# Performance work log

Hardware: AMD Instinct MI355X
Metric: run time of the kernel (lower is better)

The kernel has to match this reference:

```python
import jax, jax.numpy as jnp
import numpy as np

M = 4096   # out_features
N = 4096   # in_features
K_NNZ = 204  # nnz per row -> keep_ratio ~ 0.05
T = 8192   # tokens (batch*seq)


def setup_inputs() -> dict:
    key = jax.random.key(0)
    k1, k2, k3, k4 = jax.random.split(key, 4)
    # CSR structure: K_NNZ unique sorted columns per row (constant index buffers)
    rng = np.random.default_rng(0)
    cols = np.argsort(rng.random((M, N)), axis=1)[:, :K_NNZ]
    cols = np.sort(cols, axis=1).astype(np.int32)
    col_idx = jnp.asarray(cols.reshape(-1))                      # [nnz]
    row_ids = jnp.asarray(np.repeat(np.arange(M, dtype=np.int32), K_NNZ))  # [nnz]
    x = jax.random.normal(k1, (T, N), dtype=jnp.float32)
    dense_weight = jax.random.normal(k2, (M, N), dtype=jnp.float32) * 0.02
    bias = jax.random.normal(k3, (M,), dtype=jnp.float32) * 0.02
    sparse_values = jax.random.normal(k4, (M * K_NNZ,), dtype=jnp.float32) * 0.02
    return {"x": x, "dense_weight": dense_weight, "bias": bias,
            "sparse_values": sparse_values, "row_ids": row_ids, "col_idx": col_idx}


def reference(x, dense_weight, bias, sparse_values, row_ids, col_idx):
    # sp_add: scatter CSR values into the frozen dense weight (W = W_dense + W_sparse)
    W = dense_weight.at[row_ids, col_idx].add(sparse_values)     # [M, N]
    # sp_mm hot path: y = x @ W^T + b
    return jnp.dot(x, W.T) + bias                                # [T, M]
```

## Files before the change

kernel.cpp:

```cpp
#include <hip/hip_runtime.h>


typedef __attribute__((ext_vector_type(8))) __bf16 bf16x8;
typedef __attribute__((ext_vector_type(4))) float f32x4;
typedef __attribute__((ext_vector_type(8))) unsigned short u16x8;

#define BARRIER()   asm volatile("s_barrier" ::: "memory")
#define WAITLGKM0() asm volatile("s_waitcnt lgkmcnt(0)" ::: "memory")
#define WAITVM0()   asm volatile("s_waitcnt vmcnt(0)" ::: "memory")
#define SCHED0()    __builtin_amdgcn_sched_barrier(0)

__device__ __forceinline__ unsigned short f2bf(float f) {
  unsigned int u = __builtin_bit_cast(unsigned int, f);
  u += 0x7FFFu + ((u >> 16) & 1u);
  return (unsigned short)(u >> 16);
}

__global__ __launch_bounds__(256) void cvt_f32_bf16(
    const float* __restrict__ s, unsigned short* __restrict__ d, long n8) {
  long i = (long)blockIdx.x * blockDim.x + threadIdx.x;
  const long stride = (long)gridDim.x * blockDim.x;
  for (; i < n8; i += stride) {
    const float4* sp = (const float4*)(s + i * 8);
    float4 a = sp[0];
    float4 b = sp[1];
    u16x8 o;
    o[0] = f2bf(a.x); o[1] = f2bf(a.y); o[2] = f2bf(a.z); o[3] = f2bf(a.w);
    o[4] = f2bf(b.x); o[5] = f2bf(b.y); o[6] = f2bf(b.z); o[7] = f2bf(b.w);
    *(u16x8*)(d + i * 8) = o;
  }
}

__global__ __launch_bounds__(256) void sparse_scatter(
    const float* __restrict__ dense, const float* __restrict__ vals,
    const int* __restrict__ rows, const int* __restrict__ cols,
    unsigned short* __restrict__ Wb, int nnz, int K) {
  int i = blockIdx.x * blockDim.x + threadIdx.x;
  if (i < nnz) {
    size_t off = (size_t)rows[i] * (size_t)K + (size_t)cols[i];
    Wb[off] = f2bf(dense[off] + vals[i]);
  }
}

__global__ __launch_bounds__(512, 2) void gemm256f(
    const unsigned short* __restrict__ A,
    const unsigned short* __restrict__ B,
    const float* __restrict__ bias,
    float* __restrict__ C,
    int Tm, int Mn, int K) {
  extern __shared__ __align__(16) char smem[];

  const int tid  = threadIdx.x;
  const int lane = tid & 63;
  const int wid  = tid >> 6;
  const int wm = (wid >> 2) * 128;
  const int wn = (wid & 3) * 64;

  const int nwg = gridDim.x;
  int bid = blockIdx.x;
  if ((nwg & 7) == 0) bid = (bid & 7) * (nwg >> 3) + (bid >> 3);
  const int ntn = Mn >> 8;
  const int bm0 = (bid / ntn) << 8;
  const int bn0 = (bid % ntn) << 8;

  const int NT = K >> 6;

  const int sr  = tid >> 3;
  const int gq8 = ((tid & 7) ^ (sr & 7)) * 8;
  const unsigned short* Asrc = A + (size_t)(bm0 + sr) * K + gq8;
  const unsigned short* Bsrc = B + (size_t)(bn0 + sr) * K + gq8;
  const size_t r64 = (size_t)64 * K;
  const int ldst = tid * 16;

#define STAGEH(SRC, H, LDSB, KOFF) do {                                          \
    __builtin_amdgcn_global_load_lds(                                            \
      (const __attribute__((address_space(1))) void*)((SRC) + (size_t)(H)*2*r64 + (KOFF)), \
      (__attribute__((address_space(3))) void*)(smem + (LDSB) + ldst), 16, 0, 0);\
    __builtin_amdgcn_global_load_lds(                                            \
      (const __attribute__((address_space(1))) void*)((SRC) + (size_t)(H)*2*r64 + r64 + (KOFF)), \
      (__attribute__((address_space(3))) void*)(smem + (LDSB) + 8192 + ldst), 16, 0, 0); \
  } while (0)

  const int fr = lane & 15, cq = lane >> 4;
  const int f7 = fr & 7;
  const int q0 = ((cq ^ f7) << 4);
  const int q1 = (((4 + cq) ^ f7) << 4);
  const int arow = (wm + fr) * 128;
  const int brow = (wn + fr) * 128;

  f32x4 acc[8][4] = {};
  bf16x8 aq0[4], aq1[4], bA0[2], bA1[2], bB0[2], bB1[2];

  STAGEH(Asrc, 0, 0, 0);
  STAGEH(Asrc, 1, 16384, 0);
  STAGEH(Bsrc, 0, 32768, 0);
  STAGEH(Bsrc, 1, 49152, 0);
  WAITVM0();
  BARRIER();

#pragma unroll 2
  for (int t = 0; t < NT; ++t) {
    const char* Ab = smem + (t & 1) * 65536;
    const char* Bb = Ab + 32768;
    const int nbase = ((t & 1) ^ 1) * 65536;
    const int kn = (t + 1) * 64;

    if (t + 1 < NT) {
      STAGEH(Asrc, 0, nbase, kn);
      STAGEH(Asrc, 1, nbase + 16384, kn);
      STAGEH(Bsrc, 0, nbase + 32768, kn);
      STAGEH(Bsrc, 1, nbase + 49152, kn);
    }

#pragma unroll
    for (int m = 0; m < 4; ++m) {
      aq0[m] = *(const bf16x8*)(Ab + arow + m * 2048 + q0);
      aq1[m] = *(const bf16x8*)(Ab + arow + m * 2048 + q1);
    }
#pragma unroll
    for (int n = 0; n < 2; ++n) {
      bA0[n] = *(const bf16x8*)(Bb + brow + n * 2048 + q0);
      bA1[n] = *(const bf16x8*)(Bb + brow + n * 2048 + q1);
    }
    WAITLGKM0();
    SCHED0();
    __builtin_amdgcn_s_setprio(1);
#pragma unroll
    for (int m = 0; m < 4; ++m)
#pragma unroll
      for (int n = 0; n < 2; ++n) {
        acc[m][n] = __builtin_amdgcn_mfma_f32_16x16x32_bf16(aq0[m], bA0[n], acc[m][n], 0, 0, 0);
        acc[m][n] = __builtin_amdgcn_mfma_f32_16x16x32_bf16(aq1[m], bA1[n], acc[m][n], 0, 0, 0);
      }
    __builtin_amdgcn_s_setprio(0);
    SCHED0();

#pragma unroll
    for (int n = 0; n < 2; ++n) {
      bB0[n] = *(const bf16x8*)(Bb + brow + (n + 2) * 2048 + q0);
      bB1[n] = *(const bf16x8*)(Bb + brow + (n + 2) * 2048 + q1);
    }
    WAITLGKM0();
    SCHED0();
    __builtin_amdgcn_s_setprio(1);
#pragma unroll
    for (int m = 0; m < 4; ++m)
#pragma unroll
      for (int n = 0; n < 2; ++n) {
        acc[m][n + 2] = __builtin_amdgcn_mfma_f32_16x16x32_bf16(aq0[m], bB0[n], acc[m][n + 2], 0, 0, 0);
        acc[m][n + 2] = __builtin_amdgcn_mfma_f32_16x16x32_bf16(aq1[m], bB1[n], acc[m][n + 2], 0, 0, 0);
      }
    __builtin_amdgcn_s_setprio(0);
    SCHED0();

#pragma unroll
    for (int m = 0; m < 4; ++m) {
      aq0[m] = *(const bf16x8*)(Ab + arow + (m + 4) * 2048 + q0);
      aq1[m] = *(const bf16x8*)(Ab + arow + (m + 4) * 2048 + q1);
    }
    WAITLGKM0();
    SCHED0();
    __builtin_amdgcn_s_setprio(1);
#pragma unroll
    for (int m = 0; m < 4; ++m)
#pragma unroll
      for (int n = 0; n < 2; ++n) {
        acc[m + 4][n] = __builtin_amdgcn_mfma_f32_16x16x32_bf16(aq0[m], bA0[n], acc[m + 4][n], 0, 0, 0);
        acc[m + 4][n] = __builtin_amdgcn_mfma_f32_16x16x32_bf16(aq1[m], bA1[n], acc[m + 4][n], 0, 0, 0);
      }
    __builtin_amdgcn_s_setprio(0);
    SCHED0();

    __builtin_amdgcn_s_setprio(1);
#pragma unroll
    for (int m = 0; m < 4; ++m)
#pragma unroll
      for (int n = 0; n < 2; ++n) {
        acc[m + 4][n + 2] = __builtin_amdgcn_mfma_f32_16x16x32_bf16(aq0[m], bB0[n], acc[m + 4][n + 2], 0, 0, 0);
        acc[m + 4][n + 2] = __builtin_amdgcn_mfma_f32_16x16x32_bf16(aq1[m], bB1[n], acc[m + 4][n + 2], 0, 0, 0);
      }
    __builtin_amdgcn_s_setprio(0);
    WAITVM0();
    BARRIER();
  }
#undef STAGEH

  const int c4 = cq * 4;
#pragma unroll
  for (int n = 0; n < 4; ++n) {
    const int col = bn0 + wn + n * 16 + fr;
    const float bv = bias[col];
#pragma unroll
    for (int m = 0; m < 8; ++m) {
      const size_t rowb = (size_t)(bm0 + wm + m * 16 + c4);
#pragma unroll
      for (int q = 0; q < 4; ++q)
        C[(rowb + q) * (size_t)Mn + col] = acc[m][n][q] + bv;
    }
  }
}

extern "C" void kernel_launch(void* const* d_in, const int* in_sizes, int n_in,
                              void* d_out, int out_size, void* d_ws, size_t ws_size,
                              hipStream_t stream) {
  const float* x     = (const float*)d_in[0];
  const float* dw    = (const float*)d_in[1];
  const float* bias  = (const float*)d_in[2];
  const float* sv    = (const float*)d_in[3];
  const int*   rows  = (const int*)d_in[4];
  const int*   cols  = (const int*)d_in[5];
  float* out = (float*)d_out;

  const int  Mn = in_sizes[2];
  const long wElems = (long)in_sizes[1];
  const int  K  = (int)(wElems / Mn);
  const long xElems = (long)in_sizes[0];
  const int  Tm = (int)(xElems / K);
  const int  nnz = in_sizes[3];

  unsigned short* Wb = (unsigned short*)d_ws;
  unsigned short* Xb = Wb + wElems;

  cvt_f32_bf16<<<2048, 256, 0, stream>>>(dw, Wb, wElems / 8);
  sparse_scatter<<<(nnz + 255) / 256, 256, 0, stream>>>(dw, sv, rows, cols, Wb, nnz, K);
  cvt_f32_bf16<<<2048, 256, 0, stream>>>(x, Xb, xElems / 8);

  dim3 grid((Tm >> 8) * (Mn >> 8));
  gemm256f<<<grid, 512, 131072, stream>>>(Xb, Wb, bias, out, Tm, Mn, K);
}
```

Measured before the change: 302.5 us.

## Use four waves with 128x128 warp tiles and interleave staging with LDS reads

The GEMM workgroup drops from 8 waves to 4. Each wave now computes a 128x128 output tile with an 8x8 accumulator array, which raises register reuse per LDS fragment read. Global-to-LDS staging for the next K tile is split into A and B halves, issued between fragment reads, and the explicit lgkmcnt waits and priority hints are removed. This relies on compiler-inserted waits, and the 256 accumulator VGPRs plus fragments may push register pressure high or cause spills while halving the waves available per CU.

```diff
diff --git a/kernel.cpp b/kernel.cpp
--- a/kernel.cpp
+++ b/kernel.cpp
@@ -6,7 +6,6 @@
 typedef __attribute__((ext_vector_type(8))) unsigned short u16x8;
 
 #define BARRIER()   asm volatile("s_barrier" ::: "memory")
-#define WAITLGKM0() asm volatile("s_waitcnt lgkmcnt(0)" ::: "memory")
 #define WAITVM0()   asm volatile("s_waitcnt vmcnt(0)" ::: "memory")
 #define SCHED0()    __builtin_amdgcn_sched_barrier(0)
 
@@ -42,7 +41,7 @@
   }
 }
 
-__global__ __launch_bounds__(512, 2) void gemm256f(
+__global__ __launch_bounds__(256, 1) void gemm4w(
     const unsigned short* __restrict__ A,
     const unsigned short* __restrict__ B,
     const float* __restrict__ bias,
@@ -53,8 +52,8 @@
   const int tid  = threadIdx.x;
   const int lane = tid & 63;
   const int wid  = tid >> 6;
-  const int wm = (wid >> 2) * 128;
-  const int wn = (wid & 3) * 64;
+  const int wm = (wid >> 1) * 128;
+  const int wn = (wid & 1) * 128;
 
   const int nwg = gridDim.x;
   int bid = blockIdx.x;
@@ -69,16 +68,16 @@
   const int gq8 = ((tid & 7) ^ (sr & 7)) * 8;
   const unsigned short* Asrc = A + (size_t)(bm0 + sr) * K + gq8;
   const unsigned short* Bsrc = B + (size_t)(bn0 + sr) * K + gq8;
-  const size_t r64 = (size_t)64 * K;
+  const size_t r32 = (size_t)32 * K;
   const int ldst = tid * 16;
 
-#define STAGEH(SRC, H, LDSB, KOFF) do {                                          \
-    __builtin_amdgcn_global_load_lds(                                            \
-      (const __attribute__((address_space(1))) void*)((SRC) + (size_t)(H)*2*r64 + (KOFF)), \
-      (__attribute__((address_space(3))) void*)(smem + (LDSB) + ldst), 16, 0, 0);\
-    __builtin_amdgcn_global_load_lds(                                            \
-      (const __attribute__((address_space(1))) void*)((SRC) + (size_t)(H)*2*r64 + r64 + (KOFF)), \
-      (__attribute__((address_space(3))) void*)(smem + (LDSB) + 8192 + ldst), 16, 0, 0); \
+#define STAGE8(SRC, LDSB, KOFF) do {                                             \
+    _Pragma("unroll")                                                            \
+    for (int c = 0; c < 8; ++c)                                                  \
+      __builtin_amdgcn_global_load_lds(                                          \
+        (const __attribute__((address_space(1))) void*)((SRC) + (size_t)c * r32 + (KOFF)), \
+        (__attribute__((address_space(3))) void*)(smem + (LDSB) + c * 4096 + ldst), \
+        16, 0, 0);                                                               \
   } while (0)
 
   const int fr = lane & 15, cq = lane >> 4;
@@ -88,13 +87,11 @@
   const int arow = (wm + fr) * 128;
   const int brow = (wn + fr) * 128;
 
-  f32x4 acc[8][4] = {};
-  bf16x8 aq0[4], aq1[4], bA0[2], bA1[2], bB0[2], bB1[2];
+  f32x4 acc[8][8] = {};
+  bf16x8 a0[8], a1[8], b0[8], b1[8];
 
-  STAGEH(Asrc, 0, 0, 0);
-  STAGEH(Asrc, 1, 16384, 0);
-  STAGEH(Bsrc, 0, 32768, 0);
-  STAGEH(Bsrc, 1, 49152, 0);
+  STAGE8(Asrc, 0, 0);
+  STAGE8(Bsrc, 32768, 0);
   WAITVM0();
   BARRIER();
 
@@ -104,90 +101,51 @@
     const char* Bb = Ab + 32768;
     const int nbase = ((t & 1) ^ 1) * 65536;
     const int kn = (t + 1) * 64;
-
-    if (t + 1 < NT) {
-      STAGEH(Asrc, 0, nbase, kn);
-      STAGEH(Asrc, 1, nbase + 16384, kn);
-      STAGEH(Bsrc, 0, nbase + 32768, kn);
-      STAGEH(Bsrc, 1, nbase + 49152, kn);
-    }
+    const bool st = (t + 1 < NT);
 
 #pragma unroll
-    for (int m = 0; m < 4; ++m) {
-      aq0[m] = *(const bf16x8*)(Ab + arow + m * 2048 + q0);
-      aq1[m] = *(const bf16x8*)(Ab + arow + m * 2048 + q1);
-    }
+    for (int m = 0; m < 8; ++m)
+      a0[m] = *(const bf16x8*)(Ab + arow + m * 2048 + q0);
 #pragma unroll
-    for (int n = 0; n < 2; ++n) {
-      bA0[n] = *(const bf16x8*)(Bb + brow + n * 2048 + q0);
-      bA1[n] = *(const bf16x8*)(Bb + brow + n * 2048 + q1);
-    }
-    WAITLGKM0();
+    for (int n = 0; n < 8; ++n)
+      b0[n] = *(const bf16x8*)(Bb + brow + n * 2048 + q0);
     SCHED0();
-    __builtin_amdgcn_s_setprio(1);
-#pragma unroll
-    for (int m = 0; m < 4; ++m)
-#pragma unroll
-      for (int n = 0; n < 2; ++n) {
-        acc[m][n] = __builtin_amdgcn_mfma_f32_16x16x32_bf16(aq0[m], bA0[n], acc[m][n], 0, 0, 0);
-        acc[m][n] = __builtin_amdgcn_mfma_f32_16x16x32_bf16(aq1[m], bA1[n], acc[m][n], 0, 0, 0);
-      }
-    __builtin_amdgcn_s_setprio(0);
+
+    if (st) STAGE8(Asrc, nbase, kn);
     SCHED0();
 
 #pragma unroll
-    for (int n = 0; n < 2; ++n) {
-      bB0[n] = *(const bf16x8*)(Bb + brow + (n + 2) * 2048 + q0);
-      bB1[n] = *(const bf16x8*)(Bb + brow + (n + 2) * 2048 + q1);
-    }
-    WAITLGKM0();
+    for (int m = 0; m < 8; ++m)
+      a1[m] = *(const bf16x8*)(Ab + arow + m * 2048 + q1);
+#pragma unroll
+    for (int n = 0; n < 8; ++n)
+      b1[n] = *(const bf16x8*)(Bb + brow + n * 2048 + q1);
     SCHED0();
-    __builtin_amdgcn_s_setprio(1);
-#pragma unroll
-    for (int m = 0; m < 4; ++m)
-#pragma unroll
-      for (int n = 0; n < 2; ++n) {
-        acc[m][n + 2] = __builtin_amdgcn_mfma_f32_16x16x32_bf16(aq0[m], bB0[n], acc[m][n + 2], 0, 0, 0);
-        acc[m][n + 2] = __builtin_amdgcn_mfma_f32_16x16x32_bf16(aq1[m], bB1[n], acc[m][n + 2], 0, 0, 0);
-      }
-    __builtin_amdgcn_s_setprio(0);
+
+    if (st) STAGE8(Bsrc, nbase + 32768, kn);
     SCHED0();
 
 #pragma unroll
-    for (int m = 0; m < 4; ++m) {
-      aq0[m] = *(const bf16x8*)(Ab + arow + (m + 4) * 2048 + q0);
-      aq1[m] = *(const bf16x8*)(Ab + arow + (m + 4) * 2048 + q1);
-    }
-    WAITLGKM0();
-    SCHED0();
-    __builtin_amdgcn_s_setprio(1);
+    for (int m = 0; m < 8; ++m)
 #pragma unroll
-    for (int m = 0; m < 4; ++m)
-#pragma unroll
-      for (int n = 0; n < 2; ++n) {
-        acc[m + 4][n] = __builtin_amdgcn_mfma_f32_16x16x32_bf16(aq0[m], bA0[n], acc[m + 4][n], 0, 0, 0);
-        acc[m + 4][n] = __builtin_amdgcn_mfma_f32_16x16x32_bf16(aq1[m], bA1[n], acc[m + 4][n], 0, 0, 0);
-      }
-    __builtin_amdgcn_s_setprio(0);
+      for (int n = 0; n < 8; ++n)
+        acc[m][n] = __builtin_amdgcn_mfma_f32_16x16x32_bf16(a0[m], b0[n], acc[m][n], 0, 0, 0);
     SCHED0();
 
-    __builtin_amdgcn_s_setprio(1);
 #pragma unroll
-    for (int m = 0; m < 4; ++m)
+    for (int m = 0; m < 8; ++m)
 #pragma unroll
-      for (int n = 0; n < 2; ++n) {
-        acc[m + 4][n + 2] = __builtin_amdgcn_mfma_f32_16x16x32_bf16(aq0[m], bB0[n], acc[m + 4][n + 2], 0, 0, 0);
-        acc[m + 4][n + 2] = __builtin_amdgcn_mfma_f32_16x16x32_bf16(aq1[m], bB1[n], acc[m + 4][n + 2], 0, 0, 0);
-      }
-    __builtin_amdgcn_s_setprio(0);
+      for (int n = 0; n < 8; ++n)
+        acc[m][n] = __builtin_amdgcn_mfma_f32_16x16x32_bf16(a1[m], b1[n], acc[m][n], 0, 0, 0);
+
     WAITVM0();
     BARRIER();
   }
-#undef STAGEH
+#undef STAGE8
 
   const int c4 = cq * 4;
 #pragma unroll
-  for (int n = 0; n < 4; ++n) {
+  for (int n = 0; n < 8; ++n) {
     const int col = bn0 + wn + n * 16 + fr;
     const float bv = bias[col];
 #pragma unroll
@@ -226,5 +184,5 @@
   cvt_f32_bf16<<<2048, 256, 0, stream>>>(x, Xb, xElems / 8);
 
   dim3 grid((Tm >> 8) * (Mn >> 8));
-  gemm256f<<<grid, 512, 131072, stream>>>(Xb, Wb, bias, out, Tm, Mn, K);
+  gemm4w<<<grid, 256, 131072, stream>>>(Xb, Wb, bias, out, Tm, Mn, K);
 }
```

Result: no change. 307.3 us (+1.6%).

## Switch GEMM inner loop from 16x16x32 to 32x32x16 MFMA tiles

Applied to the files above, without the earlier changes.

Replaces the 16x16x32 bf16 MFMA fragments with 32x32x16 MFMA, so each wave holds a 4x2 grid of 32x32 accumulators over the same 128x64 wave tile. The K loop is split into four sub-steps, each loading the A and B fragments from LDS and then issuing eight MFMAs. The aim is fewer LDS reads per FLOP and fewer MFMA issues through the larger instruction shape. The cost is less interleaving of LDS loads with MFMA work, since each sub-step waits on lgkmcnt(0), and an epilogue with a different row mapping.

```diff
diff --git a/kernel.cpp b/kernel.cpp
--- a/kernel.cpp
+++ b/kernel.cpp
@@ -2,7 +2,7 @@
 
 
 typedef __attribute__((ext_vector_type(8))) __bf16 bf16x8;
-typedef __attribute__((ext_vector_type(4))) float f32x4;
+typedef __attribute__((ext_vector_type(16))) float f32x16;
 typedef __attribute__((ext_vector_type(8))) unsigned short u16x8;
 
 #define BARRIER()   asm volatile("s_barrier" ::: "memory")
@@ -42,7 +42,7 @@
   }
 }
 
-__global__ __launch_bounds__(512, 2) void gemm256f(
+__global__ __launch_bounds__(512, 2) void gemm32(
     const unsigned short* __restrict__ A,
     const unsigned short* __restrict__ B,
     const float* __restrict__ bias,
@@ -81,15 +81,14 @@
       (__attribute__((address_space(3))) void*)(smem + (LDSB) + 8192 + ldst), 16, 0, 0); \
   } while (0)
 
-  const int fr = lane & 15, cq = lane >> 4;
-  const int f7 = fr & 7;
-  const int q0 = ((cq ^ f7) << 4);
-  const int q1 = (((4 + cq) ^ f7) << 4);
-  const int arow = (wm + fr) * 128;
-  const int brow = (wn + fr) * 128;
+  const int l31 = lane & 31;
+  const int kg  = lane >> 5;
+  const int l7  = lane & 7;
+  const int arow = (wm + l31) * 128;
+  const int brow = (wn + l31) * 128;
 
-  f32x4 acc[8][4] = {};
-  bf16x8 aq0[4], aq1[4], bA0[2], bA1[2], bB0[2], bB1[2];
+  f32x16 acc[4][2] = {};
+  bf16x8 a[4], b[2];
 
   STAGEH(Asrc, 0, 0, 0);
   STAGEH(Asrc, 1, 16384, 0);
@@ -113,89 +112,44 @@
     }
 
 #pragma unroll
-    for (int m = 0; m < 4; ++m) {
-      aq0[m] = *(const bf16x8*)(Ab + arow + m * 2048 + q0);
-      aq1[m] = *(const bf16x8*)(Ab + arow + m * 2048 + q1);
+    for (int ks = 0; ks < 4; ++ks) {
+      const int qoff = (((ks << 1) + kg) ^ l7) << 4;
+#pragma unroll
+      for (int mf = 0; mf < 4; ++mf)
+        a[mf] = *(const bf16x8*)(Ab + arow + mf * 4096 + qoff);
+#pragma unroll
+      for (int nf = 0; nf < 2; ++nf)
+        b[nf] = *(const bf16x8*)(Bb + brow + nf * 4096 + qoff);
+      WAITLGKM0();
+      SCHED0();
+      __builtin_amdgcn_s_setprio(1);
+#pragma unroll
+      for (int mf = 0; mf < 4; ++mf)
+#pragma unroll
+        for (int nf = 0; nf < 2; ++nf)
+          acc[mf][nf] = __builtin_amdgcn_mfma_f32_32x32x16_bf16(
+              a[mf], b[nf], acc[mf][nf], 0, 0, 0);
+      __builtin_amdgcn_s_setprio(0);
+      SCHED0();
     }
-#pragma unroll
-    for (int n = 0; n < 2; ++n) {
-      bA0[n] = *(const bf16x8*)(Bb + brow + n * 2048 + q0);
-      bA1[n] = *(const bf16x8*)(Bb + brow + n * 2048 + q1);
-    }
-    WAITLGKM0();
-    SCHED0();
-    __builtin_amdgcn_s_setprio(1);
-#pragma unroll
-    for (int m = 0; m < 4; ++m)
-#pragma unroll
-      for (int n = 0; n < 2; ++n) {
-        acc[m][n] = __builtin_amdgcn_mfma_f32_16x16x32_bf16(aq0[m], bA0[n], acc[m][n], 0, 0, 0);
-        acc[m][n] = __builtin_amdgcn_mfma_f32_16x16x32_bf16(aq1[m], bA1[n], acc[m][n], 0, 0, 0);
-      }
-    __builtin_amdgcn_s_setprio(0);
-    SCHED0();
 
-#pragma unroll
-    for (int n = 0; n < 2; ++n) {
-      bB0[n] = *(const bf16x8*)(Bb + brow + (n + 2) * 2048 + q0);
-      bB1[n] = *(const bf16x8*)(Bb + brow + (n + 2) * 2048 + q1);
-    }
-    WAITLGKM0();
-    SCHED0();
-    __builtin_amdgcn_s_setprio(1);
-#pragma unroll
-    for (int m = 0; m < 4; ++m)
-#pragma unroll
-      for (int n = 0; n < 2; ++n) {
-        acc[m][n + 2] = __builtin_amdgcn_mfma_f32_16x16x32_bf16(aq0[m], bB0[n], acc[m][n + 2], 0, 0, 0);
-        acc[m][n + 2] = __builtin_amdgcn_mfma_f32_16x16x32_bf16(aq1[m], bB1[n], acc[m][n + 2], 0, 0, 0);
-      }
-    __builtin_amdgcn_s_setprio(0);
-    SCHED0();
-
-#pragma unroll
-    for (int m = 0; m < 4; ++m) {
-      aq0[m] = *(const bf16x8*)(Ab + arow + (m + 4) * 2048 + q0);
-      aq1[m] = *(const bf16x8*)(Ab + arow + (m + 4) * 2048 + q1);
-    }
-    WAITLGKM0();
-    SCHED0();
-    __builtin_amdgcn_s_setprio(1);
-#pragma unroll
-    for (int m = 0; m < 4; ++m)
-#pragma unroll
-      for (int n = 0; n < 2; ++n) {
-        acc[m + 4][n] = __builtin_amdgcn_mfma_f32_16x16x32_bf16(aq0[m], bA0[n], acc[m + 4][n], 0, 0, 0);
-        acc[m + 4][n] = __builtin_amdgcn_mfma_f32_16x16x32_bf16(aq1[m], bA1[n], acc[m + 4][n], 0, 0, 0);
-      }
-    __builtin_amdgcn_s_setprio(0);
-    SCHED0();
-
-    __builtin_amdgcn_s_setprio(1);
-#pragma unroll
-    for (int m = 0; m < 4; ++m)
-#pragma unroll
-      for (int n = 0; n < 2; ++n) {
-        acc[m + 4][n + 2] = __builtin_amdgcn_mfma_f32_16x16x32_bf16(aq0[m], bB0[n], acc[m + 4][n + 2], 0, 0, 0);
-        acc[m + 4][n + 2] = __builtin_amdgcn_mfma_f32_16x16x32_bf16(aq1[m], bB1[n], acc[m + 4][n + 2], 0, 0, 0);
-      }
-    __builtin_amdgcn_s_setprio(0);
     WAITVM0();
     BARRIER();
   }
 #undef STAGEH
 
-  const int c4 = cq * 4;
 #pragma unroll
-  for (int n = 0; n < 4; ++n) {
-    const int col = bn0 + wn + n * 16 + fr;
+  for (int nf = 0; nf < 2; ++nf) {
+    const int col = bn0 + wn + nf * 32 + l31;
     const float bv = bias[col];
 #pragma unroll
-    for (int m = 0; m < 8; ++m) {
-      const size_t rowb = (size_t)(bm0 + wm + m * 16 + c4);
+    for (int mf = 0; mf < 4; ++mf) {
+      const int rbase = bm0 + wm + mf * 32 + 4 * kg;
 #pragma unroll
-      for (int q = 0; q < 4; ++q)
-        C[(rowb + q) * (size_t)Mn + col] = acc[m][n][q] + bv;
+      for (int r = 0; r < 16; ++r) {
+        const int row = rbase + (r & 3) + 8 * (r >> 2);
+        C[(size_t)row * Mn + col] = acc[mf][nf][r] + bv;
+      }
     }
   }
 }
@@ -226,5 +180,5 @@
   cvt_f32_bf16<<<2048, 256, 0, stream>>>(x, Xb, xElems / 8);
 
   dim3 grid((Tm >> 8) * (Mn >> 8));
-  gemm256f<<<grid, 512, 131072, stream>>>(Xb, Wb, bias, out, Tm, Mn, K);
+  gemm32<<<grid, 512, 131072, stream>>>(Xb, Wb, bias, out, Tm, Mn, K);
 }
```

Measured after the change: 328.2 us. 1.08x slower.
